# Optimization experiments

Measured on AMD Instinct MI355X. Metric: run time of the kernel, lower is better.

Reference implementation:

```python
import jax, jax.numpy as jnp
import numpy as np

THRESHOLD = 10.0
K = 24
EPS = 1e-9
BN_EPS = 1e-5


def setup_inputs() -> dict:
    key = jax.random.key(0)
    k0, k1, k2, k3 = jax.random.split(key, 4)
    B, C, H, W = 4, 256, 64, 64
    x = jax.random.normal(k0, (B, C, H, W), jnp.float32)
    fc_w = jax.random.normal(k1, (C, C), jnp.float32) * (1.0 / np.sqrt(C))
    fc_b = jax.random.normal(k2, (C,), jnp.float32) * 0.01
    dist_w = jax.random.normal(k3, (64, C), jnp.float32) * (1.0 / np.sqrt(C))
    bn_gamma = jnp.ones((C,), jnp.float32)
    bn_beta = jnp.zeros((C,), jnp.float32)
    return {"x": x, "fc_w": fc_w, "fc_b": fc_b, "dist_w": dist_w,
            "bn_gamma": bn_gamma, "bn_beta": bn_beta}


def reference(x, fc_w, fc_b, dist_w, bn_gamma, bn_beta):
    B, C, H, W = x.shape
    N = H * W
    # ds branch: only triggers when H == 40; here H=64 so ds=1 (no pool/interp)
    x_flat = x.reshape(B, C, N).transpose(0, 2, 1)        # [B, N, C]
    # dist_embed: 1x1 conv == linear projection per spatial location
    emb = jnp.einsum('bnc,ec->bne', x_flat, dist_w)       # [B, N, 64]
    # pairwise Euclidean distances (cdist)
    sq = jnp.sum(emb * emb, axis=-1)                      # [B, N]
    d2 = sq[:, :, None] + sq[:, None, :] - 2.0 * jnp.einsum('bne,bme->bnm', emb, emb)
    dist = jnp.sqrt(jnp.clip(d2, 0.0))                    # [B, N, N]
    # kNN mask via top_k of -dist
    _, idx = jax.lax.top_k(-dist, K)                      # [B, N, K]
    bi = jnp.arange(B)[:, None, None]
    ni = jnp.arange(N)[None, :, None]
    knn_mask = jnp.zeros((B, N, N), bool).at[bi, ni, idx].set(True)
    adj = knn_mask & (dist <= THRESHOLD)
    adj = adj | jnp.eye(N, dtype=bool)[None]
    adj_f = adj.astype(x.dtype)                           # H: [B, N, E=N]
    # HypConv: X' = Dv^{-1} H De^{-1} H^T (X Theta), residual added outside
    X_lin = x_flat @ fc_w.T + fc_b                        # [B, N, C]
    Dv = jnp.clip(jnp.sum(adj_f, axis=2), EPS, None)      # [B, N]
    De = jnp.clip(jnp.sum(adj_f, axis=1), EPS, None)      # [B, E]
    H_De_inv = adj_f / De[:, None, :]
    S = (H_De_inv @ adj_f.transpose(0, 2, 1)) / Dv[:, :, None]   # [B, N, N]
    out_flat = S @ X_lin + x_flat                         # residual
    out = out_flat.transpose(0, 2, 1).reshape(B, C, H, W)
    # BatchNorm2d in training mode (batch statistics, biased variance)
    mean = jnp.mean(out, axis=(0, 2, 3))
    var = jnp.var(out, axis=(0, 2, 3))
    o = (out - mean[None, :, None, None]) * jax.lax.rsqrt(var[None, :, None, None] + BN_EPS)
    o = o * bn_gamma[None, :, None, None] + bn_beta[None, :, None, None]
    # SiLU
    return o * jax.nn.sigmoid(o)
```

## Files before the change

### kernel.cpp

```cpp
#include <hip/hip_runtime.h>

#define NB 4096
#define BATCH 4
#define CD 256
#define ED 64
#define KNN 24

typedef __attribute__((ext_vector_type(8))) short bf16x8;
typedef __attribute__((ext_vector_type(4))) float f32x4;

__device__ __forceinline__ unsigned short f2bf(float x) {
  unsigned u = __float_as_uint(x);
  unsigned r = (u + 0x7fffu + ((u >> 16) & 1u)) >> 16;
  return (unsigned short)r;
}

__global__ __launch_bounds__(256) void k_emb(const float* __restrict__ x,
                                             const float* __restrict__ dist_w,
                                             unsigned* __restrict__ emb_hl,
                                             float* __restrict__ sq,
                                             unsigned* __restrict__ thr_g) {
  __shared__ float wds[ED * CD];
  __shared__ float red[64 * 4];
  const int b = blockIdx.x >> 6;
  const int n0 = (blockIdx.x & 63) << 6;
  const int tid = threadIdx.x;
  const float4* wsrc = (const float4*)dist_w;
  float4* wdst = (float4*)wds;
#pragma unroll
  for (int k = 0; k < 16; ++k) wdst[tid + 256 * k] = wsrc[tid + 256 * k];
  __syncthreads();
  const int eg = tid >> 6;
  const int nl = tid & 63;
  const int n = n0 + nl;
  float acc[16];
#pragma unroll
  for (int t = 0; t < 16; ++t) acc[t] = 0.f;
  const float* xb = x + (size_t)b * CD * NB + n;
#pragma unroll 2
  for (int c4 = 0; c4 < CD; c4 += 4) {
    float x0 = xb[(size_t)(c4 + 0) * NB];
    float x1 = xb[(size_t)(c4 + 1) * NB];
    float x2 = xb[(size_t)(c4 + 2) * NB];
    float x3 = xb[(size_t)(c4 + 3) * NB];
#pragma unroll
    for (int t = 0; t < 16; ++t) {
      float4 wv = *(const float4*)&wds[(eg * 16 + t) * CD + c4];
      acc[t] = fmaf(x0, wv.x, acc[t]);
      acc[t] = fmaf(x1, wv.y, acc[t]);
      acc[t] = fmaf(x2, wv.z, acc[t]);
      acc[t] = fmaf(x3, wv.w, acc[t]);
    }
  }
  float s = 0.f;
#pragma unroll
  for (int t = 0; t < 16; ++t) s = fmaf(acc[t], acc[t], s);
  unsigned hw[8], lw[8];
#pragma unroll
  for (int i = 0; i < 8; ++i) {
    unsigned short h0 = f2bf(acc[2 * i]);
    unsigned short h1 = f2bf(acc[2 * i + 1]);
    float l0f = acc[2 * i] - __uint_as_float((unsigned)h0 << 16);
    float l1f = acc[2 * i + 1] - __uint_as_float((unsigned)h1 << 16);
    hw[i] = (unsigned)h0 | ((unsigned)h1 << 16);
    lw[i] = (unsigned)f2bf(l0f) | ((unsigned)f2bf(l1f) << 16);
  }
  uint4* g = (uint4*)emb_hl;
  const size_t gb = ((size_t)(b * NB + n)) * 16;
  const int k15 = n & 15;
  g[gb + ((2 * eg) ^ k15)]     = make_uint4(hw[0], hw[1], hw[2], hw[3]);
  g[gb + ((2 * eg + 1) ^ k15)] = make_uint4(hw[4], hw[5], hw[6], hw[7]);
  g[gb + ((8 + 2 * eg) ^ k15)]     = make_uint4(lw[0], lw[1], lw[2], lw[3]);
  g[gb + ((8 + 2 * eg + 1) ^ k15)] = make_uint4(lw[4], lw[5], lw[6], lw[7]);
  red[nl * 4 + eg] = s;
  __syncthreads();
  if (tid < 64) {
    sq[b * NB + n0 + tid] = red[tid * 4] + red[tid * 4 + 1] + red[tid * 4 + 2] + red[tid * 4 + 3];
    thr_g[(b << 12) + n0 + tid] = 0x42C80000u;
  }
}

__global__ __launch_bounds__(256) void k_wsplit(const float* __restrict__ fc_w,
                                                unsigned* __restrict__ w_hl) {
  const int u = blockIdx.x * 256 + threadIdx.x;
  const int c = u >> 5, cg = u & 31;
  const int kt = cg >> 3, chl = cg & 7;
  const float* src = fc_w + (size_t)c * CD + kt * 64 + chl * 8;
  unsigned hi[4], lo[4];
#pragma unroll
  for (int j = 0; j < 4; ++j) {
    float a0 = src[2 * j], a1 = src[2 * j + 1];
    unsigned short h0 = f2bf(a0), h1 = f2bf(a1);
    float l0 = a0 - __uint_as_float((unsigned)h0 << 16);
    float l1 = a1 - __uint_as_float((unsigned)h1 << 16);
    hi[j] = (unsigned)h0 | ((unsigned)h1 << 16);
    lo[j] = (unsigned)f2bf(l0) | ((unsigned)f2bf(l1) << 16);
  }
  uint4* dst = (uint4*)w_hl;
  const int base = (c * 4 + kt) * 16;
  const int k15 = c & 15;
  dst[base + (chl ^ k15)] = make_uint4(hi[0], hi[1], hi[2], hi[3]);
  dst[base + ((chl + 8) ^ k15)] = make_uint4(lo[0], lo[1], lo[2], lo[3]);
}

__global__ __launch_bounds__(512) void k_xlin(const float* __restrict__ x,
                                              const unsigned* __restrict__ w_hl,
                                              const float* __restrict__ fc_b,
                                              unsigned short* __restrict__ xlin_h) {
  __shared__ __align__(16) unsigned char smem[49152];
  float* xt = (float*)smem;
  unsigned* xhl = (unsigned*)(smem + 16384);
  unsigned* whl = (unsigned*)(smem + 32768);
  const int bid = blockIdx.x;
  const int ct = bid & 3;
  const int nt = (bid >> 2) & 63;
  const int b = bid >> 8;
  const int n0 = nt << 6;
  const int tid = threadIdx.x;
  const int w = tid >> 6, lane = tid & 63;
  const int quad = lane >> 4, lr = lane & 15;
  const int rt = w >> 1;
  const int ct0 = (w & 1) * 2;
  const int rowA = rt * 16 + lr;
  const int cvt_n = tid & 63, cvt_k8 = tid >> 6;
  uint4* whl4 = (uint4*)whl;
  uint4* xhl4 = (uint4*)xhl;
  const uint4* wg = (const uint4*)w_hl;
  f32x4 acc0 = {0.f, 0.f, 0.f, 0.f};
  f32x4 acc1 = {0.f, 0.f, 0.f, 0.f};

#pragma unroll 1
  for (int kt = 0; kt < 4; ++kt) {
    __syncthreads();
#pragma unroll
    for (int i = 0; i < 8; ++i) {
      int idx = tid + 512 * i;
      int k = idx >> 6, n = idx & 63;
      xt[k * 64 + n] = x[((size_t)(b * CD + kt * 64 + k)) * NB + n0 + n];
    }
#pragma unroll
    for (int i = 0; i < 2; ++i) {
      int idx = tid + 512 * i;
      int r = idx >> 4, ch = idx & 15;
      whl4[r * 16 + ch] = wg[(size_t)((ct * 64 + r) * 4 + kt) * 16 + ch];
    }
    __syncthreads();
    {
      unsigned hi[4], lo[4];
#pragma unroll
      for (int j = 0; j < 4; ++j) {
        float a0 = xt[(cvt_k8 * 8 + 2 * j) * 64 + cvt_n];
        float a1 = xt[(cvt_k8 * 8 + 2 * j + 1) * 64 + cvt_n];
        unsigned short h0 = f2bf(a0), h1 = f2bf(a1);
        float l0 = a0 - __uint_as_float((unsigned)h0 << 16);
        float l1 = a1 - __uint_as_float((unsigned)h1 << 16);
        hi[j] = (unsigned)h0 | ((unsigned)h1 << 16);
        lo[j] = (unsigned)f2bf(l0) | ((unsigned)f2bf(l1) << 16);
      }
      const int k15 = cvt_n & 15;
      xhl4[cvt_n * 16 + (cvt_k8 ^ k15)] = make_uint4(hi[0], hi[1], hi[2], hi[3]);
      xhl4[cvt_n * 16 + ((cvt_k8 + 8) ^ k15)] = make_uint4(lo[0], lo[1], lo[2], lo[3]);
    }
    __syncthreads();
#pragma unroll
    for (int kk = 0; kk < 2; ++kk) {
      const int cb = quad + 4 * kk;
      bf16x8 a_hi = *(const bf16x8*)&xhl[rowA * 64 + ((cb) ^ lr) * 4];
      bf16x8 a_lo = *(const bf16x8*)&xhl[rowA * 64 + ((cb + 8) ^ lr) * 4];
      int rowB0 = ct0 * 16 + lr, rowB1 = rowB0 + 16;
      bf16x8 b0_hi = *(const bf16x8*)&whl[rowB0 * 64 + ((cb) ^ lr) * 4];
      bf16x8 b0_lo = *(const bf16x8*)&whl[rowB0 * 64 + ((cb + 8) ^ lr) * 4];
      bf16x8 b1_hi = *(const bf16x8*)&whl[rowB1 * 64 + ((cb) ^ lr) * 4];
      bf16x8 b1_lo = *(const bf16x8*)&whl[rowB1 * 64 + ((cb + 8) ^ lr) * 4];
      acc0 = __builtin_amdgcn_mfma_f32_16x16x32_bf16(a_hi, b0_hi, acc0, 0, 0, 0);
      acc0 = __builtin_amdgcn_mfma_f32_16x16x32_bf16(a_hi, b0_lo, acc0, 0, 0, 0);
      acc0 = __builtin_amdgcn_mfma_f32_16x16x32_bf16(a_lo, b0_hi, acc0, 0, 0, 0);
      acc1 = __builtin_amdgcn_mfma_f32_16x16x32_bf16(a_hi, b1_hi, acc1, 0, 0, 0);
      acc1 = __builtin_amdgcn_mfma_f32_16x16x32_bf16(a_hi, b1_lo, acc1, 0, 0, 0);
      acc1 = __builtin_amdgcn_mfma_f32_16x16x32_bf16(a_lo, b1_hi, acc1, 0, 0, 0);
    }
  }
#pragma unroll
  for (int reg = 0; reg < 4; ++reg) {
    int n = n0 + rt * 16 + quad * 4 + reg;
    unsigned short* dst = xlin_h + (((size_t)(b * NB + n)) << 8) + ct * 64;
    int c0 = ct0 * 16 + lr;
    dst[c0] = f2bf(acc0[reg] + fc_b[ct * 64 + c0]);
    dst[c0 + 16] = f2bf(acc1[reg] + fc_b[ct * 64 + c0 + 16]);
  }
}

__global__ __launch_bounds__(512, 6) void k_distp(const unsigned* __restrict__ emb_hl,
                                                  const float* __restrict__ sq,
                                                  unsigned* __restrict__ thr_g,
                                                  unsigned long long* __restrict__ part) {
  __shared__ __align__(16) unsigned char smem[51968];
  unsigned* eM   = (unsigned*)smem;
  float* sqN     = (float*)(smem + 16384);
  float* sqMp    = (float*)(smem + 16640);
  unsigned* hist = (unsigned*)(smem + 18688);
  int* collectK  = (int*)(smem + 26880);
  int* cnt       = (int*)(smem + 27136);
  unsigned long long* cand = (unsigned long long*)(smem + 27392);

  const int bid = blockIdx.x;
  const int mp = bid & 7;
  const int nt = (bid >> 3) & 63;
  const int b  = bid >> 9;
  const int n0 = nt << 6;
  const int m00 = mp << 9;
  const int tid = threadIdx.x;
  const uint4* embg = (const uint4*)emb_hl;
  const size_t bbase = (size_t)b * NB;
  const int gbase = (b << 12) + n0;

  if (tid < 64) sqN[tid] = sq[b * NB + n0 + tid];
  sqMp[tid] = sq[b * NB + m00 + tid];
#pragma unroll
  for (int i = 0; i < 4; ++i) hist[tid + 512 * i] = 0;

  const int w = tid >> 6, lane = tid & 63;
  const int quad = lane >> 4, lr = lane & 15;
  const int rt = w >> 1;
  const int ct0 = (w & 1) * 2;
  const int rowA = rt * 16 + lr;
  const int rA = tid >> 4, chA = tid & 15;
  const int rB = rA + 32;

  bf16x8 aHi0 = *(const bf16x8*)&emb_hl[((bbase + n0 + rowA) * 16 + ((quad) ^ lr)) * 4];
  bf16x8 aLo0 = *(const bf16x8*)&emb_hl[((bbase + n0 + rowA) * 16 + ((quad + 8) ^ lr)) * 4];
  bf16x8 aHi1 = *(const bf16x8*)&emb_hl[((bbase + n0 + rowA) * 16 + ((quad + 4) ^ lr)) * 4];
  bf16x8 aLo1 = *(const bf16x8*)&emb_hl[((bbase + n0 + rowA) * 16 + ((quad + 12) ^ lr)) * 4];

  uint4* eM4 = (uint4*)eM;
  uint4 pf0, pf1;

#define CHUNK_MFMA_R()                                                             \
  f32x4 acc0 = {0.f, 0.f, 0.f, 0.f};                                               \
  f32x4 acc1 = {0.f, 0.f, 0.f, 0.f};                                               \
  _Pragma("unroll")                                                                \
  for (int kk = 0; kk < 2; ++kk) {                                                 \
    const int cb = quad + 4 * kk;                                                  \
    bf16x8 a_hi = kk ? aHi1 : aHi0;                                                \
    bf16x8 a_lo = kk ? aLo1 : aLo0;                                                \
    int rowB0 = ct0 * 16 + lr, rowB1 = rowB0 + 16;                                 \
    bf16x8 b0_hi = *(const bf16x8*)&eM[rowB0 * 64 + ((cb) ^ lr) * 4];              \
    bf16x8 b0_lo = *(const bf16x8*)&eM[rowB0 * 64 + ((cb + 8) ^ lr) * 4];          \
    bf16x8 b1_hi = *(const bf16x8*)&eM[rowB1 * 64 + ((cb) ^ lr) * 4];              \
    bf16x8 b1_lo = *(const bf16x8*)&eM[rowB1 * 64 + ((cb + 8) ^ lr) * 4];          \
    acc0 = __builtin_amdgcn_mfma_f32_16x16x32_bf16(a_hi, b0_hi, acc0, 0, 0, 0);    \
    acc0 = __builtin_amdgcn_mfma_f32_16x16x32_bf16(a_hi, b0_lo, acc0, 0, 0, 0);    \
    acc0 = __builtin_amdgcn_mfma_f32_16x16x32_bf16(a_lo, b0_hi, acc0, 0, 0, 0);    \
    acc1 = __builtin_amdgcn_mfma_f32_16x16x32_bf16(a_hi, b1_hi, acc1, 0, 0, 0);    \
    acc1 = __builtin_amdgcn_mfma_f32_16x16x32_bf16(a_hi, b1_lo, acc1, 0, 0, 0);    \
    acc1 = __builtin_amdgcn_mfma_f32_16x16x32_bf16(a_lo, b1_hi, acc1, 0, 0, 0);    \
  }

#define STAGE_FIRST()                                                \
  pf0 = embg[(bbase + m00 + rA) * 16 + chA];                         \
  pf1 = embg[(bbase + m00 + rB) * 16 + chA];                         \
  eM4[rA * 16 + chA] = pf0;                                          \
  eM4[rB * 16 + chA] = pf1;                                          \
  pf0 = embg[(bbase + m00 + 64 + rA) * 16 + chA];                    \
  pf1 = embg[(bbase + m00 + 64 + rB) * 16 + chA];

#define RESTAGE(ci_)                                                 \
  if ((ci_) < 7) {                                                   \
    eM4[rA * 16 + chA] = pf0;                                        \
    eM4[rB * 16 + chA] = pf1;                                        \
    if ((ci_) < 6) {                                                 \
      pf0 = embg[(bbase + m00 + ((ci_) + 2) * 64 + rA) * 16 + chA];  \
      pf1 = embg[(bbase + m00 + ((ci_) + 2) * 64 + rB) * 16 + chA];  \
    }                                                                \
  }

  STAGE_FIRST()
#pragma unroll 1
  for (int ci = 0; ci < 8; ++ci) {
    const int m0 = ci << 6;
    __syncthreads();
    CHUNK_MFMA_R()
#pragma unroll
    for (int reg = 0; reg < 4; ++reg) {
      int row = rt * 16 + quad * 4 + reg;
      int c0 = ct0 * 16 + lr, c1 = c0 + 16;
      float d20 = fmaxf(sqN[row] + sqMp[m0 + c0] - 2.f * acc0[reg], 0.f);
      float d21 = fmaxf(sqN[row] + sqMp[m0 + c1] - 2.f * acc1[reg], 0.f);
      if (__float_as_uint(d20) <= 0x42C80000u) {
        int bk0 = min(63, (int)(d20 * 0.64f));
        atomicAdd(&hist[bk0 * 32 + (row >> 1)], 1u << (16 * (row & 1)));
      }
      if (__float_as_uint(d21) <= 0x42C80000u) {
        int bk1 = min(63, (int)(d21 * 0.64f));
        atomicAdd(&hist[bk1 * 32 + (row >> 1)], 1u << (16 * (row & 1)));
      }
    }
    __syncthreads();
    RESTAGE(ci)
  }
  __syncthreads();

  if (tid < 64) {
    int cum = 0, kb = 63;
    const int sh = 16 * (tid & 1);
#pragma unroll 1
    for (int k2 = 0; k2 < 64; ++k2) {
      cum += (hist[k2 * 32 + (tid >> 1)] >> sh) & 0xFFFFu;
      if (cum >= 24) { kb = k2; break; }
    }
    float edge = (float)(kb + 2) * 1.5625f;
    atomicMin(&thr_g[gbase + tid], __float_as_uint(edge));
    unsigned tg = thr_g[gbase + tid];
    int kImp = min(63, (int)(__uint_as_float(tg) * 0.64f));
    collectK[tid] = min(kb, kImp);
    cnt[tid] = 0;
  }
#pragma unroll
  for (int i = 0; i < 6; ++i) {
    cand[tid + 512 * i] = ~0ULL;
  }
  __syncthreads();

  STAGE_FIRST()
#pragma unroll 1
  for (int ci = 0; ci < 8; ++ci) {
    const int m0 = ci << 6;
    __syncthreads();
    CHUNK_MFMA_R()
#pragma unroll
    for (int reg = 0; reg < 4; ++reg) {
      int row = rt * 16 + quad * 4 + reg;
      int c0 = ct0 * 16 + lr, c1 = c0 + 16;
      float d20 = fmaxf(sqN[row] + sqMp[m0 + c0] - 2.f * acc0[reg], 0.f);
      float d21 = fmaxf(sqN[row] + sqMp[m0 + c1] - 2.f * acc1[reg], 0.f);
      int kc = collectK[row];
      unsigned bi0 = __float_as_uint(d20), bi1 = __float_as_uint(d21);
      int bk0 = min(63, (int)(d20 * 0.64f));
      int bk1 = min(63, (int)(d21 * 0.64f));
      if (bk0 <= kc && bi0 <= 0x42C80000u) {
        int pos = atomicAdd(&cnt[row], 1);
        if (pos < 48) cand[row * 48 + pos] = ((unsigned long long)bi0 << 32) | (unsigned)(m00 + m0 + c0);
      }
      if (bk1 <= kc && bi1 <= 0x42C80000u) {
        int pos = atomicAdd(&cnt[row], 1);
        if (pos < 48) cand[row * 48 + pos] = ((unsigned long long)bi1 << 32) | (unsigned)(m00 + m0 + c1);
      }
    }
    __syncthreads();
    RESTAGE(ci)
  }
  __syncthreads();

  {
    const int row8 = tid >> 3, sub = tid & 7;
    unsigned long long last = 0;
    unsigned long long* op = part + ((size_t)bid * 64 + row8) * 24;
#pragma unroll 1
    for (int k = 0; k < 24; ++k) {
      unsigned long long lm = ~0ULL;
#pragma unroll
      for (int j2 = 0; j2 < 6; ++j2) {
        int p2 = sub + 8 * j2;
        unsigned long long v2 = cand[row8 * 48 + p2];
        if ((k == 0 || v2 > last) && v2 < lm) lm = v2;
      }
#pragma unroll
      for (int s2 = 1; s2 < 8; s2 <<= 1) {
        unsigned long long o2 = __shfl_xor(lm, s2);
        if (o2 < lm) lm = o2;
      }
      if (sub == 0) op[k] = lm;
      last = lm;
    }
  }
}

__global__ __launch_bounds__(64) void k_merge(const unsigned long long* __restrict__ part,
                                              int* __restrict__ row_idx,
                                              int* __restrict__ row_cnt,
                                              int* __restrict__ col_cnt) {
  const int row = blockIdx.x * 64 + threadIdx.x;
  const int b = row >> 12;
  const int n = row & 4095;
  const int nt = n >> 6, r = n & 63;
  const size_t gb = (size_t)(((b << 6) | nt) << 3);
  unsigned long long h[8];
  int pp[8];
#pragma unroll
  for (int t = 0; t < 8; ++t) {
    h[t] = part[((gb + t) * 64 + r) * 24];
    pp[t] = 0;
  }
  int cnt = 0;
  const int base = row * KNN;
  for (int k = 0; k < 24; ++k) {
    int bs = 0;
    unsigned long long mv = h[0];
#pragma unroll
    for (int t = 1; t < 8; ++t)
      if (h[t] < mv) { mv = h[t]; bs = t; }
    if ((unsigned)(mv >> 32) > 0x42C80000u) break;
    int mi = (int)(mv & 0xFFFFFFFFu);
    row_idx[base + cnt] = mi;
    atomicAdd(&col_cnt[(b << 12) + mi], 1);
    ++cnt;
    int np = ++pp[bs];
    h[bs] = (np < 24) ? part[((gb + bs) * 64 + r) * 24 + np] : ~0ULL;
  }
  row_cnt[row] = cnt;
#pragma unroll 4
  for (int j = cnt; j < 24; ++j) row_idx[base + j] = n;
}

__global__ __launch_bounds__(256) void k_scan(const int* __restrict__ col_cnt,
                                              int* __restrict__ col_start,
                                              int* __restrict__ col_cursor) {
  __shared__ int part[256];
  const int tid = threadIdx.x;
  const int base = tid * 64;
  int s = 0;
  for (int j = 0; j < 64; ++j) s += col_cnt[base + j];
  part[tid] = s;
  __syncthreads();
  for (int off = 1; off < 256; off <<= 1) {
    int v = (tid >= off) ? part[tid - off] : 0;
    __syncthreads();
    part[tid] += v;
    __syncthreads();
  }
  int run = part[tid] - s;
  for (int j = 0; j < 64; ++j) {
    col_start[base + j] = run;
    col_cursor[base + j] = run;
    run += col_cnt[base + j];
  }
}

__global__ __launch_bounds__(64) void k_fill(const int* __restrict__ row_idx,
                                             const int* __restrict__ row_cnt,
                                             int* __restrict__ col_cursor,
                                             int* __restrict__ col_list) {
  const int row = blockIdx.x * 64 + threadIdx.x;
  const int b = row >> 12;
  const int cnt = row_cnt[row];
  for (int j = 0; j < cnt; ++j) {
    int m = row_idx[row * KNN + j];
    int pos = atomicAdd(&col_cursor[(b << 12) + m], 1);
    col_list[pos] = row & 4095;
  }
}

__global__ __launch_bounds__(256) void k_yd(const unsigned short* __restrict__ xlin_h,
                                            const int* __restrict__ col_cnt,
                                            const int* __restrict__ col_start,
                                            const int* __restrict__ col_list,
                                            float* __restrict__ yd) {
  const int le = threadIdx.x >> 6;
  const int c4 = threadIdx.x & 63;
  const int be = blockIdx.x * 4 + le;
  const int b = be >> 12;
  const int deg = col_cnt[be];
  const int start = col_start[be];
  float4 acc = make_float4(0.f, 0.f, 0.f, 0.f);
#define BF2F_LO(u) __uint_as_float(((u) & 0xFFFFu) << 16)
#define BF2F_HI(u) __uint_as_float((u) & 0xFFFF0000u)
  int j = 0;
  for (; j + 3 < deg; j += 4) {
    int ma = col_list[start + j], mb2 = col_list[start + j + 1];
    int mc = col_list[start + j + 2], md = col_list[start + j + 3];
    uint2 va = *(const uint2*)&xlin_h[(((size_t)(b << 12) + ma) << 8) + c4 * 4];
    uint2 vb = *(const uint2*)&xlin_h[(((size_t)(b << 12) + mb2) << 8) + c4 * 4];
    uint2 vc = *(const uint2*)&xlin_h[(((size_t)(b << 12) + mc) << 8) + c4 * 4];
    uint2 vd = *(const uint2*)&xlin_h[(((size_t)(b << 12) + md) << 8) + c4 * 4];
    acc.x += (BF2F_LO(va.x) + BF2F_LO(vb.x)) + (BF2F_LO(vc.x) + BF2F_LO(vd.x));
    acc.y += (BF2F_HI(va.x) + BF2F_HI(vb.x)) + (BF2F_HI(vc.x) + BF2F_HI(vd.x));
    acc.z += (BF2F_LO(va.y) + BF2F_LO(vb.y)) + (BF2F_LO(vc.y) + BF2F_LO(vd.y));
    acc.w += (BF2F_HI(va.y) + BF2F_HI(vb.y)) + (BF2F_HI(vc.y) + BF2F_HI(vd.y));
  }
  for (; j < deg; ++j) {
    int m = col_list[start + j];
    uint2 v = *(const uint2*)&xlin_h[(((size_t)(b << 12) + m) << 8) + c4 * 4];
    acc.x += BF2F_LO(v.x); acc.y += BF2F_HI(v.x);
    acc.z += BF2F_LO(v.y); acc.w += BF2F_HI(v.y);
  }
  float inv = 1.f / (float)deg;
  acc.x *= inv; acc.y *= inv; acc.z *= inv; acc.w *= inv;
  *(float4*)&yd[((size_t)be << 8) + c4 * 4] = acc;
}

__global__ __launch_bounds__(256) void k_out2(const float* __restrict__ yd,
                                              const int* __restrict__ row_idx,
                                              const int* __restrict__ row_cnt,
                                              float* __restrict__ outf) {
  const int b = blockIdx.x >> 8;
  const int nt = blockIdx.x & 255;
  const int le = threadIdx.x >> 6;
  const int c4 = threadIdx.x & 63;
  for (int ii = 0; ii < 4; ++ii) {
    int n = nt * 16 + le * 4 + ii;
    int row = (b << 12) + n;
    int cnt = row_cnt[row];
    int idx[24];
    const int4* ip = (const int4*)(row_idx + (size_t)row * KNN);
#pragma unroll
    for (int t = 0; t < 6; ++t) {
      int4 v = ip[t];
      idx[4 * t] = v.x; idx[4 * t + 1] = v.y; idx[4 * t + 2] = v.z; idx[4 * t + 3] = v.w;
    }
    float4 acc = make_float4(0.f, 0.f, 0.f, 0.f);
#pragma unroll
    for (int j = 0; j < 24; ++j) {
      float wgt = (j < cnt) ? 1.f : 0.f;
      float4 v = *(const float4*)&yd[(((size_t)(b << 12) + idx[j]) << 8) + c4 * 4];
      acc.x = fmaf(wgt, v.x, acc.x);
      acc.y = fmaf(wgt, v.y, acc.y);
      acc.z = fmaf(wgt, v.z, acc.z);
      acc.w = fmaf(wgt, v.w, acc.w);
    }
    float inv = 1.f / (float)cnt;
    acc.x *= inv; acc.y *= inv; acc.z *= inv; acc.w *= inv;
    *(float4*)&outf[((size_t)row << 8) + c4 * 4] = acc;
  }
}

__global__ __launch_bounds__(256) void k_res_bn(const float* __restrict__ x,
                                                float* __restrict__ outf,
                                                float* __restrict__ bn_sum,
                                                float* __restrict__ bn_sumsq) {
  __shared__ float xt[256 * 69];
  const int b = blockIdx.x >> 6;
  const int n0 = (blockIdx.x & 63) << 6;
  const int tid = threadIdx.x;
#pragma unroll 4
  for (int k = 0; k < 16; ++k) {
    int q = tid + 256 * k;
    int c = q >> 4, f = q & 15;
    float4 v = *(const float4*)&x[((size_t)(b * CD + c)) * NB + n0 + 4 * f];
    xt[c * 69 + 4 * f + 0] = v.x;
    xt[c * 69 + 4 * f + 1] = v.y;
    xt[c * 69 + 4 * f + 2] = v.z;
    xt[c * 69 + 4 * f + 3] = v.w;
  }
  __syncthreads();
  float s = 0.f, q = 0.f;
  const size_t rbase = ((size_t)((b << 12) + n0)) << 8;
#pragma unroll 4
  for (int i = 0; i < 64; ++i) {
    float v = outf[rbase + (size_t)i * 256 + tid] + xt[tid * 69 + i];
    outf[rbase + (size_t)i * 256 + tid] = v;
    s += v;
    q = fmaf(v, v, q);
  }
  atomicAdd(&bn_sum[tid], s);
  atomicAdd(&bn_sumsq[tid], q);
}

__global__ __launch_bounds__(256) void k_write(const float* __restrict__ outf,
                                               const float* __restrict__ bn_sum,
                                               const float* __restrict__ bn_sumsq,
                                               const float* __restrict__ gamma,
                                               const float* __restrict__ beta,
                                               float* __restrict__ out) {
  __shared__ float tile[64 * 257];
  __shared__ float sc[256], sh[256];
  const int b = blockIdx.x >> 6;
  const int n0 = (blockIdx.x & 63) << 6;
  const int tid = threadIdx.x;
  {
    const float inv = 1.f / 16384.f;
    float mean = bn_sum[tid] * inv;
    float var = bn_sumsq[tid] * inv - mean * mean;
    float scf = gamma[tid] * rsqrtf(var + 1e-5f);
    sc[tid] = scf;
    sh[tid] = beta[tid] - mean * scf;
  }
  __syncthreads();
#pragma unroll 4
  for (int i = 0; i < 64; ++i) {
    int idx = tid + 256 * i;
    int n = idx >> 8, c = idx & 255;
    float v = outf[(((size_t)(b << 12) + n0 + n) << 8) + c];
    v = fmaf(v, sc[c], sh[c]);
    float w = v / (1.f + expf(-v));
    tile[n * 257 + c] = w;
  }
  __syncthreads();
  const int nl = tid & 63;
  const int cg = tid >> 6;
#pragma unroll 4
  for (int j = 0; j < 64; ++j) {
    int c = cg * 64 + j;
    out[((size_t)(b * CD + c)) * NB + n0 + nl] = tile[nl * 257 + c];
  }
}

extern "C" void kernel_launch(void* const* d_in, const int* in_sizes, int n_in,
                              void* d_out, int out_size, void* d_ws, size_t ws_size,
                              hipStream_t stream) {
  const float* x      = (const float*)d_in[0];
  const float* fc_w   = (const float*)d_in[1];
  const float* fc_b   = (const float*)d_in[2];
  const float* dist_w = (const float*)d_in[3];
  const float* gamma  = (const float*)d_in[4];
  const float* beta   = (const float*)d_in[5];
  float* out = (float*)d_out;
  char* ws = (char*)d_ws;

  const size_t OFF_EHL   = 0;
  const size_t OFF_XLIN  = (size_t)4 << 20;
  const size_t OFF_YD    = (size_t)20 << 20;
  const size_t OFF_OUTF  = (size_t)36 << 20;
  const size_t OFF_SQ    = (size_t)52 << 20;
  const size_t OFF_RIDX  = OFF_SQ + 65536;
  const size_t OFF_RCNT  = OFF_RIDX + 1572864;
  const size_t OFF_CCNT  = OFF_RCNT + 65536;
  const size_t OFF_CSTART = OFF_CCNT + 65536;
  const size_t OFF_CCUR  = OFF_CSTART + 65536;
  const size_t OFF_CLIST = OFF_CCUR + 65536;
  const size_t OFF_BNS   = OFF_CLIST + 1572864;
  const size_t OFF_BNQ   = OFF_BNS + 1024;
  const size_t OFF_THRG  = OFF_BNQ + 1024;
  const size_t OFF_WHL   = OFF_THRG + 65536;
  const size_t TOTAL = OFF_WHL + 262144;
  if (ws_size < TOTAL) return;

  unsigned* emb_hl = (unsigned*)(ws + OFF_EHL);
  unsigned short* xlin_h = (unsigned short*)(ws + OFF_XLIN);
  float* yd    = (float*)(ws + OFF_YD);
  float* outf  = (float*)(ws + OFF_OUTF);
  unsigned long long* part = (unsigned long long*)(ws + OFF_YD);
  float* sq    = (float*)(ws + OFF_SQ);
  int* row_idx = (int*)(ws + OFF_RIDX);
  int* row_cnt = (int*)(ws + OFF_RCNT);
  int* col_cnt = (int*)(ws + OFF_CCNT);
  int* col_start = (int*)(ws + OFF_CSTART);
  int* col_cursor = (int*)(ws + OFF_CCUR);
  int* col_list = (int*)(ws + OFF_CLIST);
  float* bn_sum = (float*)(ws + OFF_BNS);
  float* bn_sumsq = (float*)(ws + OFF_BNQ);
  unsigned* thr_g = (unsigned*)(ws + OFF_THRG);
  unsigned* w_hl = (unsigned*)(ws + OFF_WHL);

  hipMemsetAsync(col_cnt, 0, 65536, stream);
  hipMemsetAsync(bn_sum, 0, 2048, stream);

  k_emb<<<256, 256, 0, stream>>>(x, dist_w, emb_hl, sq, thr_g);
  k_wsplit<<<32, 256, 0, stream>>>(fc_w, w_hl);
  k_xlin<<<1024, 512, 0, stream>>>(x, w_hl, fc_b, xlin_h);
  k_distp<<<2048, 512, 0, stream>>>(emb_hl, sq, thr_g, part);
  k_merge<<<256, 64, 0, stream>>>(part, row_idx, row_cnt, col_cnt);
  k_scan<<<1, 256, 0, stream>>>(col_cnt, col_start, col_cursor);
  k_fill<<<256, 64, 0, stream>>>(row_idx, row_cnt, col_cursor, col_list);
  k_yd<<<4096, 256, 0, stream>>>(xlin_h, col_cnt, col_start, col_list, yd);
  k_out2<<<1024, 256, 0, stream>>>(yd, row_idx, row_cnt, outf);
  k_res_bn<<<256, 256, 0, stream>>>(x, outf, bn_sum, bn_sumsq);
  k_write<<<256, 256, 0, stream>>>(outf, bn_sum, bn_sumsq, gamma, beta, out);
}
```

Baseline: 450.4 us.

## Store intermediate yd in bf16 and fuse residual plus BN stats into k_out2

The per-edge aggregate yd is now written as bf16, which halves both its write traffic and the traffic of the 24-way gather that reads it back. The residual add and the BatchNorm sum and sum-of-squares are folded into k_out2, using an LDS tile of x and shared-memory atomics before the global atomics. This removes the k_res_bn kernel and its read-modify-write pass over outf. In exchange yd loses precision, and the x tile load uses scalar strided reads across channels.

```diff
diff --git a/kernel.cpp b/kernel.cpp
--- a/kernel.cpp
+++ b/kernel.cpp
@@ -450,11 +450,14 @@
   }
 }
 
+#define BF2F_LO(u) __uint_as_float(((u) & 0xFFFFu) << 16)
+#define BF2F_HI(u) __uint_as_float((u) & 0xFFFF0000u)
+
 __global__ __launch_bounds__(256) void k_yd(const unsigned short* __restrict__ xlin_h,
                                             const int* __restrict__ col_cnt,
                                             const int* __restrict__ col_start,
                                             const int* __restrict__ col_list,
-                                            float* __restrict__ yd) {
+                                            unsigned short* __restrict__ yd_h) {
   const int le = threadIdx.x >> 6;
   const int c4 = threadIdx.x & 63;
   const int be = blockIdx.x * 4 + le;
@@ -462,8 +465,6 @@
   const int deg = col_cnt[be];
   const int start = col_start[be];
   float4 acc = make_float4(0.f, 0.f, 0.f, 0.f);
-#define BF2F_LO(u) __uint_as_float(((u) & 0xFFFFu) << 16)
-#define BF2F_HI(u) __uint_as_float((u) & 0xFFFF0000u)
   int j = 0;
   for (; j + 3 < deg; j += 4) {
     int ma = col_list[start + j], mb2 = col_list[start + j + 1];
@@ -484,20 +485,40 @@
     acc.z += BF2F_LO(v.y); acc.w += BF2F_HI(v.y);
   }
   float inv = 1.f / (float)deg;
-  acc.x *= inv; acc.y *= inv; acc.z *= inv; acc.w *= inv;
-  *(float4*)&yd[((size_t)be << 8) + c4 * 4] = acc;
-}
-
-__global__ __launch_bounds__(256) void k_out2(const float* __restrict__ yd,
+  unsigned p0 = (unsigned)f2bf(acc.x * inv) | ((unsigned)f2bf(acc.y * inv) << 16);
+  unsigned p1 = (unsigned)f2bf(acc.z * inv) | ((unsigned)f2bf(acc.w * inv) << 16);
+  *(uint2*)&yd_h[((size_t)be << 8) + c4 * 4] = make_uint2(p0, p1);
+}
+
+__global__ __launch_bounds__(256) void k_out2(const unsigned short* __restrict__ yd_h,
                                               const int* __restrict__ row_idx,
                                               const int* __restrict__ row_cnt,
-                                              float* __restrict__ outf) {
+                                              const float* __restrict__ x,
+                                              float* __restrict__ outf,
+                                              float* __restrict__ bn_sum,
+                                              float* __restrict__ bn_sumsq) {
+  __shared__ float xt[16 * 260];
+  __shared__ float bnS[256], bnQ[256];
   const int b = blockIdx.x >> 8;
   const int nt = blockIdx.x & 255;
-  const int le = threadIdx.x >> 6;
-  const int c4 = threadIdx.x & 63;
+  const int n0g = nt * 16;
+  const int tid = threadIdx.x;
+  const int le = tid >> 6;
+  const int c4 = tid & 63;
+  bnS[tid] = 0.f;
+  bnQ[tid] = 0.f;
+#pragma unroll
+  for (int i = 0; i < 16; ++i) {
+    int idx = tid + 256 * i;
+    int c = idx >> 4, j = idx & 15;
+    xt[j * 260 + c] = x[((size_t)(b * CD + c)) * NB + n0g + j];
+  }
+  __syncthreads();
+  float4 s4 = make_float4(0.f, 0.f, 0.f, 0.f);
+  float4 q4 = make_float4(0.f, 0.f, 0.f, 0.f);
   for (int ii = 0; ii < 4; ++ii) {
-    int n = nt * 16 + le * 4 + ii;
+    int jr = le * 4 + ii;
+    int n = n0g + jr;
     int row = (b << 12) + n;
     int cnt = row_cnt[row];
     int idx[24];
@@ -511,48 +532,35 @@
 #pragma unroll
     for (int j = 0; j < 24; ++j) {
       float wgt = (j < cnt) ? 1.f : 0.f;
-      float4 v = *(const float4*)&yd[(((size_t)(b << 12) + idx[j]) << 8) + c4 * 4];
-      acc.x = fmaf(wgt, v.x, acc.x);
-      acc.y = fmaf(wgt, v.y, acc.y);
-      acc.z = fmaf(wgt, v.z, acc.z);
-      acc.w = fmaf(wgt, v.w, acc.w);
+      uint2 v = *(const uint2*)&yd_h[(((size_t)(b << 12) + idx[j]) << 8) + c4 * 4];
+      acc.x = fmaf(wgt, BF2F_LO(v.x), acc.x);
+      acc.y = fmaf(wgt, BF2F_HI(v.x), acc.y);
+      acc.z = fmaf(wgt, BF2F_LO(v.y), acc.z);
+      acc.w = fmaf(wgt, BF2F_HI(v.y), acc.w);
     }
     float inv = 1.f / (float)cnt;
-    acc.x *= inv; acc.y *= inv; acc.z *= inv; acc.w *= inv;
-    *(float4*)&outf[((size_t)row << 8) + c4 * 4] = acc;
-  }
-}
-
-__global__ __launch_bounds__(256) void k_res_bn(const float* __restrict__ x,
-                                                float* __restrict__ outf,
-                                                float* __restrict__ bn_sum,
-                                                float* __restrict__ bn_sumsq) {
-  __shared__ float xt[256 * 69];
-  const int b = blockIdx.x >> 6;
-  const int n0 = (blockIdx.x & 63) << 6;
-  const int tid = threadIdx.x;
-#pragma unroll 4
-  for (int k = 0; k < 16; ++k) {
-    int q = tid + 256 * k;
-    int c = q >> 4, f = q & 15;
-    float4 v = *(const float4*)&x[((size_t)(b * CD + c)) * NB + n0 + 4 * f];
-    xt[c * 69 + 4 * f + 0] = v.x;
-    xt[c * 69 + 4 * f + 1] = v.y;
-    xt[c * 69 + 4 * f + 2] = v.z;
-    xt[c * 69 + 4 * f + 3] = v.w;
-  }
-  __syncthreads();
-  float s = 0.f, q = 0.f;
-  const size_t rbase = ((size_t)((b << 12) + n0)) << 8;
-#pragma unroll 4
-  for (int i = 0; i < 64; ++i) {
-    float v = outf[rbase + (size_t)i * 256 + tid] + xt[tid * 69 + i];
-    outf[rbase + (size_t)i * 256 + tid] = v;
-    s += v;
-    q = fmaf(v, v, q);
-  }
-  atomicAdd(&bn_sum[tid], s);
-  atomicAdd(&bn_sumsq[tid], q);
+    float4 xv = *(const float4*)&xt[jr * 260 + 4 * c4];
+    float4 o;
+    o.x = fmaf(acc.x, inv, xv.x);
+    o.y = fmaf(acc.y, inv, xv.y);
+    o.z = fmaf(acc.z, inv, xv.z);
+    o.w = fmaf(acc.w, inv, xv.w);
+    *(float4*)&outf[((size_t)row << 8) + c4 * 4] = o;
+    s4.x += o.x; s4.y += o.y; s4.z += o.z; s4.w += o.w;
+    q4.x = fmaf(o.x, o.x, q4.x); q4.y = fmaf(o.y, o.y, q4.y);
+    q4.z = fmaf(o.z, o.z, q4.z); q4.w = fmaf(o.w, o.w, q4.w);
+  }
+  atomicAdd(&bnS[4 * c4 + 0], s4.x);
+  atomicAdd(&bnS[4 * c4 + 1], s4.y);
+  atomicAdd(&bnS[4 * c4 + 2], s4.z);
+  atomicAdd(&bnS[4 * c4 + 3], s4.w);
+  atomicAdd(&bnQ[4 * c4 + 0], q4.x);
+  atomicAdd(&bnQ[4 * c4 + 1], q4.y);
+  atomicAdd(&bnQ[4 * c4 + 2], q4.z);
+  atomicAdd(&bnQ[4 * c4 + 3], q4.w);
+  __syncthreads();
+  atomicAdd(&bn_sum[tid], bnS[tid]);
+  atomicAdd(&bn_sumsq[tid], bnQ[tid]);
 }
 
 __global__ __launch_bounds__(256) void k_write(const float* __restrict__ outf,
@@ -626,7 +634,7 @@
 
   unsigned* emb_hl = (unsigned*)(ws + OFF_EHL);
   unsigned short* xlin_h = (unsigned short*)(ws + OFF_XLIN);
-  float* yd    = (float*)(ws + OFF_YD);
+  unsigned short* yd_h = (unsigned short*)(ws + OFF_YD);
   float* outf  = (float*)(ws + OFF_OUTF);
   unsigned long long* part = (unsigned long long*)(ws + OFF_YD);
   float* sq    = (float*)(ws + OFF_SQ);
@@ -651,8 +659,7 @@
   k_merge<<<256, 64, 0, stream>>>(part, row_idx, row_cnt, col_cnt);
   k_scan<<<1, 256, 0, stream>>>(col_cnt, col_start, col_cursor);
   k_fill<<<256, 64, 0, stream>>>(row_idx, row_cnt, col_cursor, col_list);
-  k_yd<<<4096, 256, 0, stream>>>(xlin_h, col_cnt, col_start, col_list, yd);
-  k_out2<<<1024, 256, 0, stream>>>(yd, row_idx, row_cnt, outf);
-  k_res_bn<<<256, 256, 0, stream>>>(x, outf, bn_sum, bn_sumsq);
+  k_yd<<<4096, 256, 0, stream>>>(xlin_h, col_cnt, col_start, col_list, yd_h);
+  k_out2<<<1024, 256, 0, stream>>>(yd_h, row_idx, row_cnt, x, outf, bn_sum, bn_sumsq);
   k_write<<<256, 256, 0, stream>>>(outf, bn_sum, bn_sumsq, gamma, beta, out);
 }
```

After: 448.1 us. Within noise of the previous version (-0.5%).
